# Kernel optimization log

Measured on AMD Instinct MI355X. Metric: run time of the kernel, lower is better.

## Reference

```python
import jax, jax.numpy as jnp
import numpy as np

HIDDEN = 512
HEADS = 8
HEAD_DIM = HIDDEN // HEADS
D_FF = 4 * HIDDEN
NEG = -1e9


def _layernorm(x, g, b, eps=1e-5):
    mu = jnp.mean(x, axis=-1, keepdims=True)
    var = jnp.var(x, axis=-1, keepdims=True)
    return (x - mu) * jax.lax.rsqrt(var + eps) * g + b


def setup_inputs() -> dict:
    key = jax.random.key(0)
    ks = jax.random.split(key, 16)
    B, S = 2, 2048
    s = 1.0 / np.sqrt(HIDDEN)
    inp = {
        "x": jax.random.normal(ks[0], (B, S, HIDDEN), dtype=jnp.float32),
        "adj_mask": jax.random.bernoulli(ks[1], 0.5, (B, S, S)),
        "ln1_g": jnp.ones((HIDDEN,), jnp.float32),
        "ln1_b": jnp.zeros((HIDDEN,), jnp.float32),
        "ln2_g": jnp.ones((HIDDEN,), jnp.float32),
        "ln2_b": jnp.zeros((HIDDEN,), jnp.float32),
        "Wq": jax.random.uniform(ks[2], (HIDDEN, HIDDEN), jnp.float32, -s, s),
        "bq": jnp.zeros((HIDDEN,), jnp.float32),
        "Wk": jax.random.uniform(ks[3], (HIDDEN, HIDDEN), jnp.float32, -s, s),
        "bk": jnp.zeros((HIDDEN,), jnp.float32),
        "Wv": jax.random.uniform(ks[4], (HIDDEN, HIDDEN), jnp.float32, -s, s),
        "bv": jnp.zeros((HIDDEN,), jnp.float32),
        "Wo": jax.random.uniform(ks[5], (HIDDEN, HIDDEN), jnp.float32, -s, s),
        "bo": jnp.zeros((HIDDEN,), jnp.float32),
        "W1": jax.random.uniform(ks[6], (HIDDEN, D_FF), jnp.float32, -s, s),
        "b1": jnp.zeros((D_FF,), jnp.float32),
        "W2": jax.random.uniform(ks[7], (D_FF, HIDDEN), jnp.float32, -1.0 / np.sqrt(D_FF), 1.0 / np.sqrt(D_FF)),
        "b2": jnp.zeros((HIDDEN,), jnp.float32),
    }
    return inp


def reference(x, adj_mask, ln1_g, ln1_b, ln2_g, ln2_b, Wq, bq, Wk, bk, Wv, bv,
              Wo, bo, W1, b1, W2, b2):
    B, S, H = x.shape
    nx = _layernorm(x, ln1_g, ln1_b)
    q = (nx @ Wq + bq).reshape(B, S, HEADS, HEAD_DIM)
    k = (nx @ Wk + bk).reshape(B, S, HEADS, HEAD_DIM)
    v = (nx @ Wv + bv).reshape(B, S, HEADS, HEAD_DIM)
    # scores: [B, heads, S, S]
    scores = jnp.einsum('bqhd,bkhd->bhqk', q, k) / np.sqrt(HEAD_DIM)
    scores = jnp.where(adj_mask[:, None, :, :], scores, NEG)
    attn = jax.nn.softmax(scores, axis=-1)  # dropout in eval mode = identity
    out = jnp.einsum('bhqk,bkhd->bqhd', attn, v).reshape(B, S, H)
    out = out @ Wo + bo
    x = x + out
    nx = _layernorm(x, ln2_g, ln2_b)
    mlp = jax.nn.gelu(nx @ W1 + b1, approximate=False) @ W2 + b2
    return x + mlp
```

## Files before the change

### kernel.cpp

```cpp
#include <hip/hip_runtime.h>
#include <math.h>

typedef unsigned short u16;
typedef unsigned long long u64;
typedef __bf16 bf16x8 __attribute__((ext_vector_type(8)));
typedef float f32x4 __attribute__((ext_vector_type(4)));
typedef unsigned short u16x8 __attribute__((ext_vector_type(8)));
typedef unsigned short u16x4 __attribute__((ext_vector_type(4)));

#define S_LEN 2048
#define BATCH 2
#define HID 512
#define NHEAD 8
#define DHEAD 64
#define DFF 2048
#define ROWS (BATCH * S_LEN)
#define NQH (BATCH * NHEAD * S_LEN)
#define NPART 2
#define KVSPAN (S_LEN / NPART)
#define QSCALE 0.18033688011112042f

static __device__ __forceinline__ u16 f2bf(float f) {
  unsigned int u = __builtin_bit_cast(unsigned int, f);
  u += 0x7fffu + ((u >> 16) & 1u);
  return (u16)(u >> 16);
}
static __device__ __forceinline__ u16 f2bf_fast(float f) {
  return __builtin_bit_cast(u16, (__bf16)f);
}
static __device__ __forceinline__ float bf2f(u16 v) {
  return (float)__builtin_bit_cast(__bf16, v);
}

static __device__ __forceinline__ void gl16(const void* g, void* l) {
  __builtin_amdgcn_global_load_lds(
      (const __attribute__((address_space(1))) void*)g,
      (__attribute__((address_space(3))) void*)l, 16, 0, 0);
}

__global__ __launch_bounds__(256) void prep_kernel(
    const void* __restrict__ mask, const float* __restrict__ x,
    const float* __restrict__ ln1g, const float* __restrict__ ln1b,
    const float* __restrict__ Wq, const float* __restrict__ Wk,
    const float* __restrict__ Wv, const float* __restrict__ Wo,
    const float* __restrict__ W1, const float* __restrict__ W2,
    u64* __restrict__ mpk, u16* __restrict__ wqkvT, u16* __restrict__ woT,
    u16* __restrict__ w1T, u16* __restrict__ w2T, u16* __restrict__ nx) {
  __shared__ u16 sT[64][80];
  int bid = blockIdx.x, tid = threadIdx.x;
  int wid = tid >> 6, lane = tid & 63;
  if (bid < 2048) {
    const unsigned int* m32 = (const unsigned int*)mask;
    unsigned int v0 = m32[lane];
    u64 bi = __ballot(v0 > 1u);
    u64 bf = __ballot(v0 != 0u && v0 != 0x3f800000u);
    int flag = (bi == 0ull) ? 1 : ((bf == 0ull) ? 2 : 0);
    int gw = (bid * 256 + tid) >> 6;
    const int nw = 8192;
    const int nwords = ROWS * (S_LEN / 64);
    for (int wI = gw; wI < nwords; wI += nw) {
      size_t e = (size_t)wI * 64 + lane;
      bool bit;
      if (flag == 1) bit = ((const int*)mask)[e] != 0;
      else if (flag == 2) bit = ((const float*)mask)[e] != 0.f;
      else bit = ((const unsigned char*)mask)[e] != 0;
      u64 bb = __ballot(bit);
      if (lane == 0) {
        int row = wI >> 5, w = wI & 31;
        int b = row >> 11, qq = row & 2047;
        mpk[(((size_t)(b * 32 + (qq >> 6)) * 32 + w) << 6) + (qq & 63)] = bb;
      }
    }
  } else if (bid < 2816) {
    int id = bid - 2048;
    const float* W;
    u16* WT;
    int K, N, bx, by;
    if (id < 256) {
      int mat = id >> 6, sub = id & 63;
      bx = sub & 7; by = sub >> 3; K = 512; N = 512;
      W = (mat == 0) ? Wq : (mat == 1) ? Wk : (mat == 2) ? Wv : Wo;
      WT = (mat < 3) ? wqkvT + (size_t)mat * 512 * 512 : woT;
    } else if (id < 512) {
      int sub = id - 256;
      bx = sub & 31; by = sub >> 5; K = 512; N = 2048;
      W = W1; WT = w1T;
    } else {
      int sub = id - 512;
      bx = sub & 7; by = sub >> 3; K = 2048; N = 512;
      W = W2; WT = w2T;
    }
    int r = tid >> 2, c0 = (tid & 3) * 16;
    int k0 = by * 64, n0 = bx * 64;
    const float* src = W + (size_t)(k0 + r) * N + n0 + c0;
    u16x8 a, b;
#pragma unroll
    for (int j = 0; j < 8; ++j) a[j] = f2bf(src[j]);
#pragma unroll
    for (int j = 0; j < 8; ++j) b[j] = f2bf(src[8 + j]);
    *(u16x8*)&sT[r][c0] = a;
    *(u16x8*)&sT[r][c0 + 8] = b;
    __syncthreads();
    u16x8 o0, o1;
#pragma unroll
    for (int j = 0; j < 8; ++j) o0[j] = sT[c0 + j][r];
#pragma unroll
    for (int j = 0; j < 8; ++j) o1[j] = sT[c0 + 8 + j][r];
    u16* dst = WT + (size_t)(n0 + r) * K + k0 + c0;
    *(u16x8*)dst = o0;
    *(u16x8*)(dst + 8) = o1;
  } else {
    long row = (long)(bid - 2816) * 4 + wid;
    const float* xr = x + row * HID;
    float4 v0 = *(const float4*)(xr + lane * 8);
    float4 v1 = *(const float4*)(xr + lane * 8 + 4);
    float fr[8] = {v0.x, v0.y, v0.z, v0.w, v1.x, v1.y, v1.z, v1.w};
    float s = 0.f, q = 0.f;
#pragma unroll
    for (int j = 0; j < 8; ++j) { s += fr[j]; q += fr[j] * fr[j]; }
#pragma unroll
    for (int mby = 1; mby < 64; mby <<= 1) {
      s += __shfl_xor(s, mby);
      q += __shfl_xor(q, mby);
    }
    float mean = s * (1.f / HID);
    float var = q * (1.f / HID) - mean * mean;
    float rs = rsqrtf(var + 1e-5f);
    u16x8 ov;
#pragma unroll
    for (int j = 0; j < 8; ++j) {
      int c = lane * 8 + j;
      ov[j] = f2bf((fr[j] - mean) * rs * ln1g[c] + ln1b[c]);
    }
    *(u16x8*)(nx + row * HID + lane * 8) = ov;
  }
}

__global__ __launch_bounds__(256) void ln_kernel(const float* __restrict__ x,
                                                 const float* __restrict__ g,
                                                 const float* __restrict__ b,
                                                 u16* __restrict__ o) {
  int wid = threadIdx.x >> 6, lane = threadIdx.x & 63;
  long row = (long)blockIdx.x * 4 + wid;
  const float* xr = x + row * HID;
  float4 v0 = *(const float4*)(xr + lane * 8);
  float4 v1 = *(const float4*)(xr + lane * 8 + 4);
  float fr[8] = {v0.x, v0.y, v0.z, v0.w, v1.x, v1.y, v1.z, v1.w};
  float s = 0.f, q = 0.f;
#pragma unroll
  for (int j = 0; j < 8; ++j) { s += fr[j]; q += fr[j] * fr[j]; }
#pragma unroll
  for (int mby = 1; mby < 64; mby <<= 1) {
    s += __shfl_xor(s, mby);
    q += __shfl_xor(q, mby);
  }
  float mean = s * (1.f / HID);
  float var = q * (1.f / HID) - mean * mean;
  float rs = rsqrtf(var + 1e-5f);
  u16x8 ov;
#pragma unroll
  for (int j = 0; j < 8; ++j) {
    int c = lane * 8 + j;
    ov[j] = f2bf((fr[j] - mean) * rs * g[c] + b[c]);
  }
  *(u16x8*)(o + row * HID + lane * 8) = ov;
}

template <int BM, int BN, int EPI>
__global__ __launch_bounds__(256) void gemm3_kernel(
    const u16* __restrict__ A, const u16* __restrict__ BT,
    const float* __restrict__ bias, const float* __restrict__ bias2,
    const float* __restrict__ bias3, const float* __restrict__ resid,
    void* __restrict__ o1, void* __restrict__ o2, void* __restrict__ o3,
    int M, int N, int K) {
  constexpr int AM = BM / 32;
  constexpr int BNF = BN / 32;
  __shared__ alignas(16) u16 sA[BM * 64];
  __shared__ alignas(16) u16 sB[BN * 64];
  int tid = threadIdx.x, wid = tid >> 6, lane = tid & 63;
  int wm = wid >> 1, wn = wid & 1;
  int grp = lane >> 4, l16 = lane & 15;
  int m0 = blockIdx.y * BM, n0 = blockIdx.x * BN;
  f32x4 zz = {0.f, 0.f, 0.f, 0.f};
  f32x4 acc[AM][BNF];
#pragma unroll
  for (int i = 0; i < AM; ++i)
#pragma unroll
    for (int j = 0; j < BNF; ++j) acc[i][j] = zz;

  for (int k0 = 0; k0 < K; k0 += 64) {
#pragma unroll
    for (int i = 0; i < BM / 32; ++i) {
      int bb = i * 4096 + tid * 16;
      int row = bb >> 7;
      int cb = (bb & 127) ^ ((row & 7) << 4);
      gl16((const char*)A + ((size_t)(m0 + row) * K + k0) * 2 + cb,
           (char*)sA + i * 4096 + wid * 1024);
    }
#pragma unroll
    for (int i = 0; i < BN / 32; ++i) {
      int bb = i * 4096 + tid * 16;
      int row = bb >> 7;
      int cb = (bb & 127) ^ ((row & 7) << 4);
      gl16((const char*)BT + ((size_t)(n0 + row) * K + k0) * 2 + cb,
           (char*)sB + i * 4096 + wid * 1024);
    }
    __syncthreads();
    bf16x8 af[AM][2], bfr[BNF][2];
#pragma unroll
    for (int am = 0; am < AM; ++am) {
      int row = wm * (BM / 2) + am * 16 + l16;
#pragma unroll
      for (int kk = 0; kk < 2; ++kk)
        af[am][kk] = *(const bf16x8*)((const char*)sA + row * 128 +
                                      ((kk * 64 + grp * 16) ^ ((row & 7) << 4)));
    }
#pragma unroll
    for (int bn = 0; bn < BNF; ++bn) {
      int row = wn * (BN / 2) + bn * 16 + l16;
#pragma unroll
      for (int kk = 0; kk < 2; ++kk)
        bfr[bn][kk] = *(const bf16x8*)((const char*)sB + row * 128 +
                                       ((kk * 64 + grp * 16) ^ ((row & 7) << 4)));
    }
#pragma unroll
    for (int kk = 0; kk < 2; ++kk)
#pragma unroll
      for (int am = 0; am < AM; ++am)
#pragma unroll
        for (int bn = 0; bn < BNF; ++bn)
          acc[am][bn] = __builtin_amdgcn_mfma_f32_16x16x32_bf16(
              af[am][kk], bfr[bn][kk], acc[am][bn], 0, 0, 0);
    __syncthreads();
  }

#pragma unroll
  for (int am = 0; am < AM; ++am) {
#pragma unroll
    for (int bn = 0; bn < BNF; ++bn) {
      int gc = n0 + wn * (BN / 2) + bn * 16 + l16;
      long gr0 = m0 + wm * (BM / 2) + am * 16 + grp * 4;
      if constexpr (EPI == 0) {
        int bidx = (int)(gr0 >> 11), s0 = (int)(gr0 & 2047);
        if (gc < 512) {
          float bsv = bias[gc];
#pragma unroll
          for (int r = 0; r < 4; ++r)
            ((u16*)o1)[(size_t)(gr0 + r) * 512 + gc] =
                f2bf((acc[am][bn][r] + bsv) * QSCALE);
        } else if (gc < 1024) {
          int c = gc - 512, hh = c >> 6, d = c & 63;
          float bsv = bias2[c];
#pragma unroll
          for (int r = 0; r < 4; ++r)
            ((u16*)o2)[((size_t)(bidx * NHEAD + hh) * S_LEN + s0 + r) * 64 + d] =
                f2bf(acc[am][bn][r] + bsv);
        } else {
          int c = gc - 1024, hh = c >> 6, d = c & 63;
          float bsv = bias3[c];
          u16x4 pk;
#pragma unroll
          for (int r = 0; r < 4; ++r) pk[r] = f2bf(acc[am][bn][r] + bsv);
          *(u16x4*)((u16*)o3 +
                    (((size_t)(bidx * NHEAD + hh) * 32 + (s0 >> 6)) * 64 + d) * 64 +
                    (s0 & 63)) = pk;
        }
      } else if constexpr (EPI == 1) {
        float bsv = bias[gc];
        float* O = (float*)o1;
#pragma unroll
        for (int r = 0; r < 4; ++r) {
          size_t off = (size_t)(gr0 + r) * N + gc;
          O[off] = resid[off] + acc[am][bn][r] + bsv;
        }
      } else {
        float bsv = bias[gc];
        u16* O = (u16*)o1;
#pragma unroll
        for (int r = 0; r < 4; ++r) {
          float v = acc[am][bn][r] + bsv;
          O[(size_t)(gr0 + r) * N + gc] =
              f2bf(0.5f * v * (1.f + erff(v * 0.70710678118f)));
        }
      }
    }
  }
}

__global__ __launch_bounds__(256) void oproj_kernel(
    const u16* __restrict__ pbuf, const float2* __restrict__ mlb,
    const u16* __restrict__ BT, const float* __restrict__ bias,
    const float* __restrict__ resid, float* __restrict__ out) {
  __shared__ alignas(16) u16 sA[64 * 64];
  __shared__ alignas(16) u16 sB[64 * 64];
  int tid = threadIdx.x, wid = tid >> 6, lane = tid & 63;
  int wm = wid >> 1, wn = wid & 1;
  int grp = lane >> 4, l16 = lane & 15;
  int m0 = blockIdx.y * 64, n0 = blockIdx.x * 64;
  f32x4 zz = {0.f, 0.f, 0.f, 0.f};
  f32x4 acc[2][2] = {{zz, zz}, {zz, zz}};
  int ar = tid >> 2, ac = (tid & 3) * 16;
  int grow = m0 + ar;
  int bB = grow >> 11, q = grow & 2047;
  int rbase = bB * NHEAD * S_LEN + q;

  for (int k0 = 0; k0 < 512; k0 += 64) {
#pragma unroll
    for (int i = 0; i < 2; ++i) {
      int bb = i * 4096 + tid * 16;
      int row = bb >> 7;
      int cb = (bb & 127) ^ ((row & 7) << 4);
      gl16((const char*)BT + ((size_t)(n0 + row) * 512 + k0) * 2 + cb,
           (char*)sB + i * 4096 + wid * 1024);
    }
    int ridx = rbase + (k0 >> 6) * S_LEN;
    float2 ml0 = mlb[ridx], ml1 = mlb[NQH + ridx];
    float M = fmaxf(ml0.x, ml1.x);
    float w0 = __builtin_amdgcn_exp2f(ml0.x - M);
    float w1 = __builtin_amdgcn_exp2f(ml1.x - M);
    float rden = 1.f / (w0 * ml0.y + w1 * ml1.y);
    w0 *= rden; w1 *= rden;
    u16x8 p0a = *(const u16x8*)(pbuf + (size_t)ridx * 64 + ac);
    u16x8 p0b = *(const u16x8*)(pbuf + (size_t)ridx * 64 + ac + 8);
    u16x8 p1a = *(const u16x8*)(pbuf + ((size_t)NQH + ridx) * 64 + ac);
    u16x8 p1b = *(const u16x8*)(pbuf + ((size_t)NQH + ridx) * 64 + ac + 8);
    u16x8 oa_, ob_;
#pragma unroll
    for (int j = 0; j < 8; ++j) {
      oa_[j] = f2bf_fast(w0 * bf2f(p0a[j]) + w1 * bf2f(p1a[j]));
      ob_[j] = f2bf_fast(w0 * bf2f(p0b[j]) + w1 * bf2f(p1b[j]));
    }
    char* dst = (char*)sA + ar * 128;
    int xr_ = (ar & 7) << 4;
    *(u16x8*)(dst + ((ac * 2) ^ xr_)) = oa_;
    *(u16x8*)(dst + ((ac * 2 + 16) ^ xr_)) = ob_;
    __syncthreads();
    bf16x8 af[2][2], bfr[2][2];
#pragma unroll
    for (int am = 0; am < 2; ++am) {
      int row = wm * 32 + am * 16 + l16;
#pragma unroll
      for (int kk = 0; kk < 2; ++kk)
        af[am][kk] = *(const bf16x8*)((const char*)sA + row * 128 +
                                      ((kk * 64 + grp * 16) ^ ((row & 7) << 4)));
    }
#pragma unroll
    for (int bn = 0; bn < 2; ++bn) {
      int row = wn * 32 + bn * 16 + l16;
#pragma unroll
      for (int kk = 0; kk < 2; ++kk)
        bfr[bn][kk] = *(const bf16x8*)((const char*)sB + row * 128 +
                                       ((kk * 64 + grp * 16) ^ ((row & 7) << 4)));
    }
#pragma unroll
    for (int kk = 0; kk < 2; ++kk)
#pragma unroll
      for (int am = 0; am < 2; ++am)
#pragma unroll
        for (int bn = 0; bn < 2; ++bn)
          acc[am][bn] = __builtin_amdgcn_mfma_f32_16x16x32_bf16(
              af[am][kk], bfr[bn][kk], acc[am][bn], 0, 0, 0);
    __syncthreads();
  }

#pragma unroll
  for (int am = 0; am < 2; ++am) {
#pragma unroll
    for (int bn = 0; bn < 2; ++bn) {
      int gc = n0 + wn * 32 + bn * 16 + l16;
      long gr0 = m0 + wm * 32 + am * 16 + grp * 4;
      float bsv = bias[gc];
#pragma unroll
      for (int r = 0; r < 4; ++r) {
        size_t off = (size_t)(gr0 + r) * 512 + gc;
        out[off] = resid[off] + acc[am][bn][r] + bsv;
      }
    }
  }
}

__global__ __launch_bounds__(256, 4) void attn_kernel(
    const u16* __restrict__ qg, const u16* __restrict__ khp,
    const u16* __restrict__ vtp, const u64* __restrict__ mpk,
    u16* __restrict__ pout, float2* __restrict__ mlb) {
  __shared__ alignas(16) char sKV[2][2][8192];
  __shared__ alignas(16) u16 sP[4][16][64];
  int tid = threadIdx.x;
  int wid = tid >> 6, lane = tid & 63;
  int grp = lane >> 4, l16 = lane & 15;
  int flat = blockIdx.x;
  int swz = (flat & 7) * 128 + (flat >> 3);
  int qblk = swz & 31, part = (swz >> 5) & 1, h = (swz >> 6) & 7, b = swz >> 9;
  int q0 = qblk * 64 + wid * 16;
  int q = q0 + l16;
  const u16* qp = qg + (size_t)(b * S_LEN + q) * HID + h * DHEAD + grp * 8;
  bf16x8 qf0 = *(const bf16x8*)qp;
  bf16x8 qf1 = *(const bf16x8*)(qp + 32);
  f32x4 zz = {0.f, 0.f, 0.f, 0.f};
  f32x4 oa[4] = {zz, zz, zz, zz};
  float mr = -1e30f, lr = 0.f;
  int hh = b * NHEAD + h;
  const char* kbase = (const char*)(khp + (size_t)hh * S_LEN * DHEAD);
  const char* vbase = (const char*)(vtp + (size_t)hh * S_LEN * DHEAD);
  const u64* mbase = mpk + (((size_t)(b * 32 + qblk) * 32) << 6) + wid * 16 + l16;
  int kvb = part * KVSPAN;

  auto stage = [&](int bsel, int kv0) {
#pragma unroll
    for (int i = 0; i < 4; ++i) {
      int idx = wid * 4 + i;
      int sel = idx >> 3, j = idx & 7;
      int bb = j * 1024 + lane * 16;
      int row = bb >> 7;
      int cb = (bb & 127) ^ ((row & 7) << 4);
      const char* src =
          (sel ? vbase + ((size_t)(kv0 >> 6) << 13) : kbase + (size_t)kv0 * 128) +
          (bb & ~127) + cb;
      gl16(src, &sKV[bsel][sel][j * 1024]);
    }
  };

  stage(0, kvb);
  u64 mw = mbase[(size_t)(kvb >> 6) << 6];
  __syncthreads();
  int buf = 0;
  char* sprow = (char*)sP + wid * 2048 + l16 * 128;
  int xw = (l16 & 7) << 4;

  for (int t = 0; t < KVSPAN / 64; ++t, buf ^= 1) {
    int kv0 = kvb + t * 64;
    if (t + 1 < KVSPAN / 64) stage(buf ^ 1, kv0 + 64);
    u64 mw_next = mbase[(size_t)((kv0 >> 6) + 1) << 6];
    const char* Kb = sKV[buf][0];
    const char* Vb = sKV[buf][1];
    bf16x8 kf[4][2];
#pragma unroll
    for (int nb = 0; nb < 4; ++nb) {
      int row = nb * 16 + l16;
      int x = (row & 7) << 4;
      kf[nb][0] = *(const bf16x8*)(Kb + row * 128 + ((grp * 16) ^ x));
      kf[nb][1] = *(const bf16x8*)(Kb + row * 128 + ((64 + grp * 16) ^ x));
    }
    bf16x8 vf[2][4];
#pragma unroll
    for (int ks = 0; ks < 2; ++ks)
#pragma unroll
      for (int db = 0; db < 4; ++db) {
        int row = db * 16 + l16;
        int x = (row & 7) << 4;
        vf[ks][db] =
            *(const bf16x8*)(Vb + row * 128 + ((ks * 64 + grp * 16) ^ x));
      }
    f32x4 st[4];
#pragma unroll
    for (int nb = 0; nb < 4; ++nb) {
      f32x4 s = zz;
      s = __builtin_amdgcn_mfma_f32_16x16x32_bf16(kf[nb][0], qf0, s, 0, 0, 0);
      s = __builtin_amdgcn_mfma_f32_16x16x32_bf16(kf[nb][1], qf1, s, 0, 0, 0);
      st[nb] = s;
    }
    float tmx = -1e30f;
#pragma unroll
    for (int nb = 0; nb < 4; ++nb)
#pragma unroll
      for (int r = 0; r < 4; ++r) {
        int kbit = nb * 16 + grp * 4 + r;
        float s = ((mw >> kbit) & 1ull) ? st[nb][r] : -1e9f;
        st[nb][r] = s;
        tmx = fmaxf(tmx, s);
      }
    mw = mw_next;
    tmx = fmaxf(tmx, __shfl_xor(tmx, 16));
    tmx = fmaxf(tmx, __shfl_xor(tmx, 32));
    if (__any(tmx > mr + 4.f)) {
      float mnew = fmaxf(mr, tmx);
      float sc = __builtin_amdgcn_exp2f(mr - mnew);
      lr *= sc;
#pragma unroll
      for (int db = 0; db < 4; ++db)
#pragma unroll
        for (int r = 0; r < 4; ++r) oa[db][r] *= sc;
      mr = mnew;
    }
    float tsum = 0.f;
#pragma unroll
    for (int nb = 0; nb < 4; ++nb) {
      u16x4 pk;
#pragma unroll
      for (int r = 0; r < 4; ++r) {
        float p = __builtin_amdgcn_exp2f(st[nb][r] - mr);
        tsum += p;
        pk[r] = f2bf_fast(p);
      }
      *(u16x4*)(sprow + ((nb * 32 + grp * 8) ^ xw)) = pk;
    }
    tsum += __shfl_xor(tsum, 16);
    tsum += __shfl_xor(tsum, 32);
    lr += tsum;
    asm volatile("s_waitcnt lgkmcnt(0)" ::: "memory");
    __builtin_amdgcn_s_setprio(1);
#pragma unroll
    for (int ks = 0; ks < 2; ++ks) {
      bf16x8 pb = *(const bf16x8*)(sprow + ((ks * 64 + grp * 16) ^ xw));
#pragma unroll
      for (int db = 0; db < 4; ++db)
        oa[db] = __builtin_amdgcn_mfma_f32_16x16x32_bf16(vf[ks][db], pb, oa[db],
                                                         0, 0, 0);
    }
    __builtin_amdgcn_s_setprio(0);
    __syncthreads();
  }

#pragma unroll
  for (int db = 0; db < 4; ++db) {
    u16x4 pk;
#pragma unroll
    for (int r = 0; r < 4; ++r) pk[r] = f2bf_fast(oa[db][r]);
    *(u16x4*)(sprow + ((db * 32 + grp * 8) ^ xw)) = pk;
  }
  asm volatile("s_waitcnt lgkmcnt(0)" ::: "memory");
  int rrow = lane >> 3, rcolb = (lane & 7) * 16;
  const char* spw = (const char*)sP + wid * 2048;
  u16x8 o0 = *(const u16x8*)(spw + rrow * 128 + (rcolb ^ ((rrow & 7) << 4)));
  u16x8 o1 =
      *(const u16x8*)(spw + (8 + rrow) * 128 + (rcolb ^ ((rrow & 7) << 4)));
  int ridx0 = hh * S_LEN + q0;
  u16* pp = pout + ((size_t)part * NQH + ridx0) * 64;
  __builtin_nontemporal_store(o0, (u16x8*)(pp + lane * 8));
  __builtin_nontemporal_store(o1, (u16x8*)(pp + 512 + lane * 8));
  if (grp == 0)
    mlb[(size_t)part * NQH + ridx0 + l16] = make_float2(mr, lr);
}

extern "C" void kernel_launch(void* const* d_in, const int* in_sizes, int n_in,
                              void* d_out, int out_size, void* d_ws,
                              size_t ws_size, hipStream_t stream) {
  const float* x = (const float*)d_in[0];
  const void* mask = d_in[1];
  const float* ln1g = (const float*)d_in[2];
  const float* ln1b = (const float*)d_in[3];
  const float* ln2g = (const float*)d_in[4];
  const float* ln2b = (const float*)d_in[5];
  const float* Wq = (const float*)d_in[6];
  const float* bq = (const float*)d_in[7];
  const float* Wk = (const float*)d_in[8];
  const float* bk = (const float*)d_in[9];
  const float* Wv = (const float*)d_in[10];
  const float* bvp = (const float*)d_in[11];
  const float* Wo = (const float*)d_in[12];
  const float* bo = (const float*)d_in[13];
  const float* W1 = (const float*)d_in[14];
  const float* b1 = (const float*)d_in[15];
  const float* W2 = (const float*)d_in[16];
  const float* b2 = (const float*)d_in[17];

  char* w = (char*)d_ws;
  char* base = w + 256;
  u64* mpk = (u64*)base;
  float2* mlb = (float2*)(base + 1048576);
  u16* wqkvT = (u16*)(base + 2097152);
  u16* woT = wqkvT + 1536 * 512;
  u16* w1T = woT + 512 * 512;
  u16* w2T = w1T + 2048 * 512;
  u16* nx = (u16*)(base + 8388608);
  u16* nx2 = nx;
  u16* qb = (u16*)(base + 12582912);
  float* x2 = (float*)(base + 12582912);
  u16* khp = (u16*)(base + 16777216);
  u16* vtp = (u16*)(base + 20971520);
  u16* pbuf = (u16*)(base + 25165824);
  u16* hb = (u16*)(base + 25165824);

  prep_kernel<<<3840, 256, 0, stream>>>(mask, x, ln1g, ln1b, Wq, Wk, Wv, Wo,
                                        W1, W2, mpk, wqkvT, woT, w1T, w2T, nx);
  gemm3_kernel<128, 64, 0><<<dim3(24, 32), 256, 0, stream>>>(
      nx, wqkvT, bq, bk, bvp, nullptr, qb, khp, vtp, ROWS, 1536, HID);
  attn_kernel<<<1024, 256, 0, stream>>>(qb, khp, vtp, mpk, pbuf, mlb);
  oproj_kernel<<<dim3(8, 64), 256, 0, stream>>>(pbuf, mlb, woT, bo, x, x2);
  ln_kernel<<<1024, 256, 0, stream>>>(x2, ln2g, ln2b, nx2);
  gemm3_kernel<128, 64, 2><<<dim3(32, 32), 256, 0, stream>>>(
      nx2, w1T, b1, nullptr, nullptr, nullptr, hb, nullptr, nullptr, ROWS, DFF,
      HID);
  gemm3_kernel<64, 64, 1><<<dim3(8, 64), 256, 0, stream>>>(
      hb, w2T, b2, nullptr, nullptr, x2, d_out, nullptr, nullptr, ROWS, 512,
      DFF);
}
```

Measured before the change: 132.2 us.

## Double-buffer GEMM LDS tiles and compute softmax row sums via MFMA

The GEMM kernel now uses two LDS buffers per operand. It prefetches the next K tile with async global-to-LDS loads while the current tile is consumed, synchronising with explicit vmcnt waits and raw barriers. In the attention kernel, the per-row sum of probabilities is computed by an extra MFMA against a vector of bf16 ones instead of scalar adds and cross-lane shuffles. The max reduction is also reorganised into a tree. The risks are doubled GEMM LDS use, which may cut occupancy, and a row sum taken from bf16-rounded probabilities.

```diff
diff --git a/kernel.cpp b/kernel.cpp
--- a/kernel.cpp
+++ b/kernel.cpp
@@ -175,8 +175,9 @@
     int M, int N, int K) {
   constexpr int AM = BM / 32;
   constexpr int BNF = BN / 32;
-  __shared__ alignas(16) u16 sA[BM * 64];
-  __shared__ alignas(16) u16 sB[BN * 64];
+  constexpr int NLD = BM / 32 + BN / 32;
+  __shared__ alignas(16) u16 sA[2][BM * 64];
+  __shared__ alignas(16) u16 sB[2][BN * 64];
   int tid = threadIdx.x, wid = tid >> 6, lane = tid & 63;
   int wm = wid >> 1, wn = wid & 1;
   int grp = lane >> 4, l16 = lane & 15;
@@ -188,14 +189,14 @@
 #pragma unroll
     for (int j = 0; j < BNF; ++j) acc[i][j] = zz;
 
-  for (int k0 = 0; k0 < K; k0 += 64) {
+  auto stageAB = [&](int bsel, int k0) {
 #pragma unroll
     for (int i = 0; i < BM / 32; ++i) {
       int bb = i * 4096 + tid * 16;
       int row = bb >> 7;
       int cb = (bb & 127) ^ ((row & 7) << 4);
       gl16((const char*)A + ((size_t)(m0 + row) * K + k0) * 2 + cb,
-           (char*)sA + i * 4096 + wid * 1024);
+           (char*)sA[bsel] + i * 4096 + wid * 1024);
     }
 #pragma unroll
     for (int i = 0; i < BN / 32; ++i) {
@@ -203,25 +204,43 @@
       int row = bb >> 7;
       int cb = (bb & 127) ^ ((row & 7) << 4);
       gl16((const char*)BT + ((size_t)(n0 + row) * K + k0) * 2 + cb,
-           (char*)sB + i * 4096 + wid * 1024);
-    }
-    __syncthreads();
+           (char*)sB[bsel] + i * 4096 + wid * 1024);
+    }
+  };
+
+  stageAB(0, 0);
+  int buf = 0;
+  for (int k0 = 0; k0 < K; k0 += 64, buf ^= 1) {
+    if (k0 + 64 < K) {
+      stageAB(buf ^ 1, k0 + 64);
+      if constexpr (NLD == 6)
+        asm volatile("s_waitcnt vmcnt(6)" ::: "memory");
+      else if constexpr (NLD == 4)
+        asm volatile("s_waitcnt vmcnt(4)" ::: "memory");
+      else
+        asm volatile("s_waitcnt vmcnt(8)" ::: "memory");
+    } else {
+      asm volatile("s_waitcnt vmcnt(0)" ::: "memory");
+    }
+    __builtin_amdgcn_s_barrier();
     bf16x8 af[AM][2], bfr[BNF][2];
 #pragma unroll
     for (int am = 0; am < AM; ++am) {
       int row = wm * (BM / 2) + am * 16 + l16;
 #pragma unroll
       for (int kk = 0; kk < 2; ++kk)
-        af[am][kk] = *(const bf16x8*)((const char*)sA + row * 128 +
-                                      ((kk * 64 + grp * 16) ^ ((row & 7) << 4)));
+        af[am][kk] =
+            *(const bf16x8*)((const char*)sA[buf] + row * 128 +
+                             ((kk * 64 + grp * 16) ^ ((row & 7) << 4)));
     }
 #pragma unroll
     for (int bn = 0; bn < BNF; ++bn) {
       int row = wn * (BN / 2) + bn * 16 + l16;
 #pragma unroll
       for (int kk = 0; kk < 2; ++kk)
-        bfr[bn][kk] = *(const bf16x8*)((const char*)sB + row * 128 +
-                                       ((kk * 64 + grp * 16) ^ ((row & 7) << 4)));
+        bfr[bn][kk] =
+            *(const bf16x8*)((const char*)sB[buf] + row * 128 +
+                             ((kk * 64 + grp * 16) ^ ((row & 7) << 4)));
     }
 #pragma unroll
     for (int kk = 0; kk < 2; ++kk)
@@ -231,7 +250,8 @@
         for (int bn = 0; bn < BNF; ++bn)
           acc[am][bn] = __builtin_amdgcn_mfma_f32_16x16x32_bf16(
               af[am][kk], bfr[bn][kk], acc[am][bn], 0, 0, 0);
-    __syncthreads();
+    asm volatile("s_waitcnt lgkmcnt(0)" ::: "memory");
+    __builtin_amdgcn_s_barrier();
   }
 
 #pragma unroll
@@ -396,9 +416,13 @@
   const u16* qp = qg + (size_t)(b * S_LEN + q) * HID + h * DHEAD + grp * 8;
   bf16x8 qf0 = *(const bf16x8*)qp;
   bf16x8 qf1 = *(const bf16x8*)(qp + 32);
+  u16x8 ones_u = {0x3F80, 0x3F80, 0x3F80, 0x3F80,
+                  0x3F80, 0x3F80, 0x3F80, 0x3F80};
+  bf16x8 onesv = __builtin_bit_cast(bf16x8, ones_u);
   f32x4 zz = {0.f, 0.f, 0.f, 0.f};
   f32x4 oa[4] = {zz, zz, zz, zz};
-  float mr = -1e30f, lr = 0.f;
+  f32x4 oa_l = zz;
+  float mr = -1e30f;
   int hh = b * NHEAD + h;
   const char* kbase = (const char*)(khp + (size_t)hh * S_LEN * DHEAD);
   const char* vbase = (const char*)(vtp + (size_t)hh * S_LEN * DHEAD);
@@ -459,49 +483,44 @@
       s = __builtin_amdgcn_mfma_f32_16x16x32_bf16(kf[nb][1], qf1, s, 0, 0, 0);
       st[nb] = s;
     }
-    float tmx = -1e30f;
-#pragma unroll
-    for (int nb = 0; nb < 4; ++nb)
+    float mnb[4];
+#pragma unroll
+    for (int nb = 0; nb < 4; ++nb) {
 #pragma unroll
       for (int r = 0; r < 4; ++r) {
         int kbit = nb * 16 + grp * 4 + r;
-        float s = ((mw >> kbit) & 1ull) ? st[nb][r] : -1e9f;
-        st[nb][r] = s;
-        tmx = fmaxf(tmx, s);
+        st[nb][r] = ((mw >> kbit) & 1ull) ? st[nb][r] : -1e9f;
       }
+      mnb[nb] = fmaxf(fmaxf(fmaxf(st[nb][0], st[nb][1]), st[nb][2]), st[nb][3]);
+    }
     mw = mw_next;
+    float tmx = fmaxf(fmaxf(fmaxf(mnb[0], mnb[1]), mnb[2]), mnb[3]);
     tmx = fmaxf(tmx, __shfl_xor(tmx, 16));
     tmx = fmaxf(tmx, __shfl_xor(tmx, 32));
     if (__any(tmx > mr + 4.f)) {
       float mnew = fmaxf(mr, tmx);
       float sc = __builtin_amdgcn_exp2f(mr - mnew);
-      lr *= sc;
+      oa_l[0] *= sc; oa_l[1] *= sc; oa_l[2] *= sc; oa_l[3] *= sc;
 #pragma unroll
       for (int db = 0; db < 4; ++db)
 #pragma unroll
         for (int r = 0; r < 4; ++r) oa[db][r] *= sc;
       mr = mnew;
     }
-    float tsum = 0.f;
 #pragma unroll
     for (int nb = 0; nb < 4; ++nb) {
       u16x4 pk;
 #pragma unroll
-      for (int r = 0; r < 4; ++r) {
-        float p = __builtin_amdgcn_exp2f(st[nb][r] - mr);
-        tsum += p;
-        pk[r] = f2bf_fast(p);
-      }
+      for (int r = 0; r < 4; ++r)
+        pk[r] = f2bf_fast(__builtin_amdgcn_exp2f(st[nb][r] - mr));
       *(u16x4*)(sprow + ((nb * 32 + grp * 8) ^ xw)) = pk;
     }
-    tsum += __shfl_xor(tsum, 16);
-    tsum += __shfl_xor(tsum, 32);
-    lr += tsum;
     asm volatile("s_waitcnt lgkmcnt(0)" ::: "memory");
     __builtin_amdgcn_s_setprio(1);
 #pragma unroll
     for (int ks = 0; ks < 2; ++ks) {
       bf16x8 pb = *(const bf16x8*)(sprow + ((ks * 64 + grp * 16) ^ xw));
+      oa_l = __builtin_amdgcn_mfma_f32_16x16x32_bf16(onesv, pb, oa_l, 0, 0, 0);
 #pragma unroll
       for (int db = 0; db < 4; ++db)
         oa[db] = __builtin_amdgcn_mfma_f32_16x16x32_bf16(vf[ks][db], pb, oa[db],
@@ -529,7 +548,7 @@
   __builtin_nontemporal_store(o0, (u16x8*)(pp + lane * 8));
   __builtin_nontemporal_store(o1, (u16x8*)(pp + 512 + lane * 8));
   if (grp == 0)
-    mlb[(size_t)part * NQH + ridx0 + l16] = make_float2(mr, lr);
+    mlb[(size_t)part * NQH + ridx0 + l16] = make_float2(mr, oa_l[0]);
 }
 
 extern "C" void kernel_launch(void* const* d_in, const int* in_sizes, int n_in,
```

Result: slower. 135.3 us (+2.4%).

## Split attention KV range into four partitions and single-buffer KV tiles

Applied to the files above, without the earlier changes.

Doubles the number of KV split partitions in the attention kernel, so it launches twice as many blocks, each handling half the KV span. The output projection now merges four partial softmax results instead of two. KV staging drops from double to single buffering, and launch bounds are raised to six blocks per CU, trading prefetch overlap for higher occupancy. Mask bit extraction is also switched to 32-bit halves. The cost is twice the partial-output traffic written and then read back in the merge step, and the loss of copy/compute overlap inside each block.

```diff
diff --git a/kernel.cpp b/kernel.cpp
--- a/kernel.cpp
+++ b/kernel.cpp
@@ -16,7 +16,7 @@
 #define DFF 2048
 #define ROWS (BATCH * S_LEN)
 #define NQH (BATCH * NHEAD * S_LEN)
-#define NPART 2
+#define NPART 4
 #define KVSPAN (S_LEN / NPART)
 #define QSCALE 0.18033688011112042f
 
@@ -314,21 +314,40 @@
            (char*)sB + i * 4096 + wid * 1024);
     }
     int ridx = rbase + (k0 >> 6) * S_LEN;
-    float2 ml0 = mlb[ridx], ml1 = mlb[NQH + ridx];
-    float M = fmaxf(ml0.x, ml1.x);
-    float w0 = __builtin_amdgcn_exp2f(ml0.x - M);
-    float w1 = __builtin_amdgcn_exp2f(ml1.x - M);
-    float rden = 1.f / (w0 * ml0.y + w1 * ml1.y);
-    w0 *= rden; w1 *= rden;
-    u16x8 p0a = *(const u16x8*)(pbuf + (size_t)ridx * 64 + ac);
-    u16x8 p0b = *(const u16x8*)(pbuf + (size_t)ridx * 64 + ac + 8);
-    u16x8 p1a = *(const u16x8*)(pbuf + ((size_t)NQH + ridx) * 64 + ac);
-    u16x8 p1b = *(const u16x8*)(pbuf + ((size_t)NQH + ridx) * 64 + ac + 8);
+    float2 ml[NPART];
+    float M = -1e30f;
+#pragma unroll
+    for (int i = 0; i < NPART; ++i) {
+      ml[i] = mlb[(size_t)i * NQH + ridx];
+      M = fmaxf(M, ml[i].x);
+    }
+    float wgt[NPART], wsum = 0.f;
+#pragma unroll
+    for (int i = 0; i < NPART; ++i) {
+      wgt[i] = __builtin_amdgcn_exp2f(ml[i].x - M);
+      wsum += wgt[i] * ml[i].y;
+    }
+    float rden = 1.f / wsum;
+#pragma unroll
+    for (int i = 0; i < NPART; ++i) wgt[i] *= rden;
+    float va[8] = {0, 0, 0, 0, 0, 0, 0, 0};
+    float vb[8] = {0, 0, 0, 0, 0, 0, 0, 0};
+#pragma unroll
+    for (int i = 0; i < NPART; ++i) {
+      const u16* pp = pbuf + ((size_t)i * NQH + ridx) * 64 + ac;
+      u16x8 pa = *(const u16x8*)pp;
+      u16x8 pb_ = *(const u16x8*)(pp + 8);
+#pragma unroll
+      for (int j = 0; j < 8; ++j) {
+        va[j] += wgt[i] * bf2f(pa[j]);
+        vb[j] += wgt[i] * bf2f(pb_[j]);
+      }
+    }
     u16x8 oa_, ob_;
 #pragma unroll
     for (int j = 0; j < 8; ++j) {
-      oa_[j] = f2bf_fast(w0 * bf2f(p0a[j]) + w1 * bf2f(p1a[j]));
-      ob_[j] = f2bf_fast(w0 * bf2f(p0b[j]) + w1 * bf2f(p1b[j]));
+      oa_[j] = f2bf_fast(va[j]);
+      ob_[j] = f2bf_fast(vb[j]);
     }
     char* dst = (char*)sA + ar * 128;
     int xr_ = (ar & 7) << 4;
@@ -379,18 +398,18 @@
   }
 }
 
-__global__ __launch_bounds__(256, 4) void attn_kernel(
+__global__ __launch_bounds__(256, 6) void attn_kernel(
     const u16* __restrict__ qg, const u16* __restrict__ khp,
     const u16* __restrict__ vtp, const u64* __restrict__ mpk,
     u16* __restrict__ pout, float2* __restrict__ mlb) {
-  __shared__ alignas(16) char sKV[2][2][8192];
+  __shared__ alignas(16) char sKV[2][8192];
   __shared__ alignas(16) u16 sP[4][16][64];
   int tid = threadIdx.x;
   int wid = tid >> 6, lane = tid & 63;
   int grp = lane >> 4, l16 = lane & 15;
   int flat = blockIdx.x;
-  int swz = (flat & 7) * 128 + (flat >> 3);
-  int qblk = swz & 31, part = (swz >> 5) & 1, h = (swz >> 6) & 7, b = swz >> 9;
+  int swz = (flat & 7) * 256 + (flat >> 3);
+  int qblk = swz & 31, part = (swz >> 5) & 3, h = (swz >> 7) & 7, b = swz >> 10;
   int q0 = qblk * 64 + wid * 16;
   int q = q0 + l16;
   const u16* qp = qg + (size_t)(b * S_LEN + q) * HID + h * DHEAD + grp * 8;
@@ -405,7 +424,7 @@
   const u64* mbase = mpk + (((size_t)(b * 32 + qblk) * 32) << 6) + wid * 16 + l16;
   int kvb = part * KVSPAN;
 
-  auto stage = [&](int bsel, int kv0) {
+  auto stage = [&](int kv0) {
 #pragma unroll
     for (int i = 0; i < 4; ++i) {
       int idx = wid * 4 + i;
@@ -416,23 +435,20 @@
       const char* src =
           (sel ? vbase + ((size_t)(kv0 >> 6) << 13) : kbase + (size_t)kv0 * 128) +
           (bb & ~127) + cb;
-      gl16(src, &sKV[bsel][sel][j * 1024]);
+      gl16(src, &sKV[sel][j * 1024]);
     }
   };
 
-  stage(0, kvb);
-  u64 mw = mbase[(size_t)(kvb >> 6) << 6];
-  __syncthreads();
-  int buf = 0;
   char* sprow = (char*)sP + wid * 2048 + l16 * 128;
   int xw = (l16 & 7) << 4;
 
-  for (int t = 0; t < KVSPAN / 64; ++t, buf ^= 1) {
+  for (int t = 0; t < KVSPAN / 64; ++t) {
     int kv0 = kvb + t * 64;
-    if (t + 1 < KVSPAN / 64) stage(buf ^ 1, kv0 + 64);
-    u64 mw_next = mbase[(size_t)((kv0 >> 6) + 1) << 6];
-    const char* Kb = sKV[buf][0];
-    const char* Vb = sKV[buf][1];
+    stage(kv0);
+    u64 mw = mbase[(size_t)(kv0 >> 6) << 6];
+    __syncthreads();
+    const char* Kb = sKV[0];
+    const char* Vb = sKV[1];
     bf16x8 kf[4][2];
 #pragma unroll
     for (int nb = 0; nb < 4; ++nb) {
@@ -459,17 +475,19 @@
       s = __builtin_amdgcn_mfma_f32_16x16x32_bf16(kf[nb][1], qf1, s, 0, 0, 0);
       st[nb] = s;
     }
+    unsigned mlo = (unsigned)mw, mhi = (unsigned)(mw >> 32);
     float tmx = -1e30f;
 #pragma unroll
-    for (int nb = 0; nb < 4; ++nb)
+    for (int nb = 0; nb < 4; ++nb) {
+      unsigned msel = (nb < 2) ? mlo : mhi;
+      int bb0 = (nb & 1) * 16 + grp * 4;
 #pragma unroll
       for (int r = 0; r < 4; ++r) {
-        int kbit = nb * 16 + grp * 4 + r;
-        float s = ((mw >> kbit) & 1ull) ? st[nb][r] : -1e9f;
+        float s = ((msel >> (bb0 + r)) & 1u) ? st[nb][r] : -1e9f;
         st[nb][r] = s;
         tmx = fmaxf(tmx, s);
       }
-    mw = mw_next;
+    }
     tmx = fmaxf(tmx, __shfl_xor(tmx, 16));
     tmx = fmaxf(tmx, __shfl_xor(tmx, 32));
     if (__any(tmx > mr + 4.f)) {
@@ -575,7 +593,7 @@
                                         W1, W2, mpk, wqkvT, woT, w1T, w2T, nx);
   gemm3_kernel<128, 64, 0><<<dim3(24, 32), 256, 0, stream>>>(
       nx, wqkvT, bq, bk, bvp, nullptr, qb, khp, vtp, ROWS, 1536, HID);
-  attn_kernel<<<1024, 256, 0, stream>>>(qb, khp, vtp, mpk, pbuf, mlb);
+  attn_kernel<<<2048, 256, 0, stream>>>(qb, khp, vtp, mpk, pbuf, mlb);
   oproj_kernel<<<dim3(8, 64), 256, 0, stream>>>(pbuf, mlb, woT, bo, x, x2);
   ln_kernel<<<1024, 256, 0, stream>>>(x2, ln2g, ln2b, nx2);
   gemm3_kernel<128, 64, 2><<<dim3(32, 32), 256, 0, stream>>>(
```

New measurement: 186.7 us. 1.41x slower.
